# Kernel tuning notes

Hardware: AMD Instinct MI355X
Metric: run time of the kernel (lower is better)

The kernel has to match this reference:

```python
import jax, jax.numpy as jnp
import numpy as np
import math

B, H, N, L = 8, 512, 64, 4096

def setup_inputs() -> dict:
    key = jax.random.key(0)
    k = jax.random.split(key, 8)
    u = jax.random.normal(k[0], (B, H, L), dtype=jnp.float32)
    log_dt = jax.random.uniform(k[1], (H,), dtype=jnp.float32) * (math.log(0.1) - math.log(0.001)) + math.log(0.001)
    C_re = jax.random.normal(k[2], (H, N // 2), dtype=jnp.float32)
    C_im = jax.random.normal(k[3], (H, N // 2), dtype=jnp.float32)
    log_A_real = jnp.log(0.5 * jnp.ones((H, N // 2), dtype=jnp.float32))
    A_imag = math.pi * jnp.broadcast_to(jnp.arange(N // 2, dtype=jnp.float32), (H, N // 2))
    D = jax.random.normal(k[4], (H,), dtype=jnp.float32)
    # 1x1 conv H -> 2H (weights stored (2H, H)), PyTorch-like init scale 1/sqrt(H)
    s = 1.0 / math.sqrt(H)
    W = jax.random.uniform(k[5], (2 * H, H), dtype=jnp.float32, minval=-s, maxval=s)
    b = jax.random.uniform(k[6], (2 * H,), dtype=jnp.float32, minval=-s, maxval=s)
    return {"u": u, "log_dt": log_dt, "C_re": C_re, "C_im": C_im,
            "log_A_real": log_A_real, "A_imag": A_imag, "D": D, "W": W, "b": b}

def reference(u, log_dt, C_re, C_im, log_A_real, A_imag, D, W, b):
    Lq = u.shape[-1]
    dt = jnp.exp(log_dt)                       # (H,)
    C = C_re + 1j * C_im                       # (H, N/2)
    A = -jnp.exp(log_A_real) + 1j * A_imag     # (H, N/2)
    dtA = A * dt[:, None]                      # (H, N/2)
    # Vandermonde: exp(dtA * l) for l in [0, L)
    Kv = jnp.exp(dtA[:, :, None] * jnp.arange(Lq, dtype=jnp.float32))  # (H, N/2, L)
    Ck = C * (jnp.exp(dtA) - 1.0) / A          # (H, N/2)
    k = 2.0 * jnp.einsum('hn,hnl->hl', Ck, Kv).real  # (H, L)
    # FFT-based causal convolution with length-2L zero padding
    k_f = jnp.fft.rfft(k, n=2 * Lq)            # (H, L+1)
    u_f = jnp.fft.rfft(u, n=2 * Lq)            # (B, H, L+1)
    y = jnp.fft.irfft(u_f * k_f, n=2 * Lq)[..., :Lq]  # (B, H, L)
    y = y + u * D[:, None]
    y = jax.nn.gelu(y, approximate=False)      # nn.GELU default (erf)
    # 1x1 conv H -> 2H then GLU over channel dim (-2)
    z = jnp.einsum('oh,bhl->bol', W, y) + b[:, None]   # (B, 2H, L)
    a, g = jnp.split(z, 2, axis=-2)
    return a * jax.nn.sigmoid(g)               # (B, H, L)
```

## Files before the change

### kernel.cpp

```cpp
#include <hip/hip_runtime.h>
#include <hip/hip_bf16.h>
#include <math.h>

#define Bb 8
#define Hh 512
#define N2 32
#define Ll 4096
#define CH 256
#define NCH 16

#define KG_OFF  8388608
#define CKR_OFF (KG_OFF + 131072)
#define CKI_OFF (CKR_OFF + 16384)
#define W256R_OFF (CKI_OFF + 16384)
#define W256I_OFF (W256R_OFF + 16384)
#define WNHI_OFF 18874368u
#define WNLO_OFF 27525120u

typedef short bf16x8 __attribute__((ext_vector_type(8)));
typedef float f32x4  __attribute__((ext_vector_type(4)));

__device__ __forceinline__ float gelu_f(float x) {
    return 0.5f * x * (1.f + erff(x * 0.70710678118654752f));
}
__device__ __forceinline__ unsigned short f2bf(float f) {
    __hip_bfloat16 h = __float2bfloat16(f);
    return *reinterpret_cast<unsigned short*>(&h);
}
__device__ __forceinline__ float bf2f(unsigned short s) {
    return __uint_as_float(((unsigned int)s) << 16);
}

__global__ __launch_bounds__(256) void s4d_k1(
    const float* __restrict__ log_dt,
    const float* __restrict__ C_re,  const float* __restrict__ C_im,
    const float* __restrict__ log_A_real, const float* __restrict__ A_imag,
    const float* __restrict__ W,
    float* __restrict__ scratch, unsigned short* __restrict__ Wb,
    unsigned short* __restrict__ wnhi, unsigned short* __restrict__ wnlo,
    unsigned short* __restrict__ wnt)
{
    __shared__ __align__(16) float wLr[N2][257];
    __shared__ __align__(16) float wLi[N2][257];
    __shared__ float Ck2r[N2], Ck2i[N2];

    const int tid = threadIdx.x;
    const int h = blockIdx.x;

    {
        const int i4 = (blockIdx.x * 256 + tid) * 4;
        const float4 wv = *(const float4*)&W[i4];
        unsigned short o[4] = {f2bf(wv.x), f2bf(wv.y), f2bf(wv.z), f2bf(wv.w)};
        *(uint2*)&Wb[i4] = *(uint2*)o;
    }

    const float dt = expf(log_dt[h]);
    const int n = tid & 31, tq = tid >> 5;

    const float lar = log_A_real[h * N2 + n];
    const float Aim = A_imag[h * N2 + n];
    const float Are = -expf(lar);
    const float dar = Are * dt, dai = Aim * dt;

    float wr, wi;
    { float e = expf(dar); float sn, cs; sincosf(dai, &sn, &cs); wr = e * cs; wi = e * sn; }
    const float j0 = (float)(32 * tq + 1);
    float cr, ci;
    { float e = expf(dar * j0); float sn, cs; sincosf(dai * j0, &sn, &cs); cr = e * cs; ci = e * sn; }
    #pragma unroll 8
    for (int i = 0; i < 32; ++i) {
        const int j = 32 * tq + i;
        wLr[n][j] = cr; wLi[n][j] = ci;
        const float tr = cr * wr - ci * wi;
        ci = cr * wi + ci * wr; cr = tr;
    }

    if (tid < N2) {
        const float er = wr - 1.f, ei = wi;
        const float den = Are * Are + Aim * Aim;
        const float qr = (er * Are + ei * Aim) / den;
        const float qi = (ei * Are - er * Aim) / den;
        const float c_r = C_re[h * N2 + tid], c_i = C_im[h * N2 + tid];
        const float k2r = 2.f * (c_r * qr - c_i * qi);
        const float k2i = 2.f * (c_r * qi + c_i * qr);
        Ck2r[tid] = k2r; Ck2i[tid] = k2i;
        scratch[CKR_OFF + h * 32 + tid] = k2r;
        scratch[CKI_OFF + h * 32 + tid] = k2i;
    }
    __syncthreads();

    {
        const int t = tid;
        float kv = 0.f;
        if (t == 0) {
            #pragma unroll
            for (int m = 0; m < N2; ++m) kv += Ck2r[m];
        } else {
            #pragma unroll
            for (int m = 0; m < N2; ++m)
                kv += Ck2r[m] * wLr[m][t - 1] - Ck2i[m] * wLi[m][t - 1];
        }
        scratch[KG_OFF + h * CH + t] = kv;
    }

    {
        unsigned short* WH  = wnhi + (size_t)h * (64 * 264);
        unsigned short* WLo = wnlo + (size_t)h * (64 * 136);
        unsigned short* WT  = wnt  + (size_t)h * (257 * 64);

        for (int idx = tid; idx < 64 * 33; idx += 256) {
            const int r = idx / 33, g = idx - 33 * r;
            const float* src = (r & 1) ? wLi[r >> 1] : wLr[r >> 1];
            __align__(16) unsigned short o[8];
            #pragma unroll
            for (int jj = 0; jj < 8; ++jj) {
                const int j = 8 * g + jj;
                const float v = (j == 0) ? ((r & 1) ? 0.f : 1.f)
                              : (j <= 256 ? src[j - 1] : 0.f);
                o[jj] = f2bf(v);
            }
            *(uint4*)&WH[r * 264 + 8 * g] = *(const uint4*)o;
        }
        for (int idx = tid; idx < 64 * 17; idx += 256) {
            const int r = idx / 17, g = idx - 17 * r;
            const float* src = (r & 1) ? wLi[r >> 1] : wLr[r >> 1];
            __align__(16) unsigned short o[8];
            #pragma unroll
            for (int jj = 0; jj < 8; ++jj) {
                const int j = 8 * g + jj;
                const float v = (j == 0) ? ((r & 1) ? 0.f : 1.f)
                              : (j < 128 ? src[j - 1] : 0.f);
                o[jj] = f2bf(v - bf2f(f2bf(v)));
            }
            *(uint4*)&WLo[r * 136 + 8 * g] = *(const uint4*)o;
        }
        for (int idx = tid; idx < 257 * 8; idx += 256) {
            const int t = idx >> 3, g = idx & 7;
            __align__(16) unsigned short o[8];
            #pragma unroll
            for (int rr = 0; rr < 8; ++rr) {
                const int r = 8 * g + rr;
                const float v = (t == 0) ? ((r & 1) ? 0.f : 1.f)
                              : ((r & 1) ? wLi[r >> 1][t - 1] : wLr[r >> 1][t - 1]);
                o[rr] = f2bf(v);
            }
            *(uint4*)&WT[t * 64 + 8 * g] = *(const uint4*)o;
        }
        if (tid < N2) {
            scratch[W256R_OFF + h * 32 + tid] = wLr[tid][255];
            scratch[W256I_OFF + h * 32 + tid] = wLi[tid][255];
        }
    }
}

__global__ __launch_bounds__(256, 3) void s4d_k23(
    const float* __restrict__ u,
    const float* __restrict__ Dp,
    const float* scratch,
    const unsigned short* wnhi, const unsigned short* wnlo,
    const unsigned short* wnt,
    unsigned short* y_bf)
{
    __shared__ __align__(16) unsigned short uhi[16 * 264];
    __shared__ __align__(16) unsigned short ulo[16 * 264];
    __shared__ __align__(16) unsigned short khi[8 * 520];
    __shared__ __align__(16) unsigned short klo[8 * 520];
    __shared__ __align__(16) float Plds[64 * 20];
    __shared__ __align__(16) unsigned short CkAhi[16 * 72];
    __shared__ __align__(16) unsigned short CkAlo[16 * 72];

    const int tid = threadIdx.x;
    const int h = blockIdx.x & (Hh - 1);
    const int b = blockIdx.x >> 9;
    const int wv = tid >> 6;
    const int lane = tid & 63;
    const int l15 = lane & 15;
    const int quad = lane >> 4;

    {
        unsigned int* z1 = (unsigned int*)khi;
        unsigned int* z2 = (unsigned int*)klo;
        for (int i = tid; i < 2080; i += 256) { z1[i] = 0; z2[i] = 0; }
    }
    const float* ub = u + (size_t)(b * Hh + h) * Ll;
    #pragma unroll
    for (int q = 0; q < 4; ++q) {
        const int l = q * 1024 + tid * 4;
        const float4 v = *(const float4*)&ub[l];
        const int c = l >> 8, s = l & 255;
        const unsigned short h3 = f2bf(v.w), h2 = f2bf(v.z), h1 = f2bf(v.y), h0 = f2bf(v.x);
        uint2 dh;
        dh.x = (unsigned int)h3 | ((unsigned int)h2 << 16);
        dh.y = (unsigned int)h1 | ((unsigned int)h0 << 16);
        *(uint2*)&uhi[c * 264 + (252 - s)] = dh;
        uint2 dl;
        dl.x = (unsigned int)f2bf(v.w - bf2f(h3)) | ((unsigned int)f2bf(v.z - bf2f(h2)) << 16);
        dl.y = (unsigned int)f2bf(v.y - bf2f(h1)) | ((unsigned int)f2bf(v.x - bf2f(h0)) << 16);
        *(uint2*)&ulo[c * 264 + (252 - s)] = dl;
    }
    const float kval = scratch[KG_OFF + h * CH + tid];
    const unsigned short k_hi = f2bf(kval);
    const unsigned short k_lo = f2bf(kval - bf2f(k_hi));
    __syncthreads();

    #pragma unroll
    for (int r = 0; r < 8; ++r) {
        const int x = tid + 255 - r;
        khi[r * 520 + x] = k_hi;
        klo[r * 520 + x] = k_lo;
    }
    {
        const unsigned short* WH = wnhi + (size_t)h * (64 * 264);
        const unsigned short* WL = wnlo + (size_t)h * (64 * 136);
        f32x4 accP = {0.f, 0.f, 0.f, 0.f};
        const int wrow = 16 * wv + l15;
        #pragma unroll
        for (int j0 = 0; j0 < 256; j0 += 32) {
            const bf16x8 ah = *(const bf16x8*)&uhi[l15 * 264 + j0 + 8 * quad];
            const bf16x8 al = *(const bf16x8*)&ulo[l15 * 264 + j0 + 8 * quad];
            const bf16x8 wh = *(const bf16x8*)&WH[wrow * 264 + j0 + 8 * quad];
            accP = __builtin_amdgcn_mfma_f32_16x16x32_bf16(ah, wh, accP, 0, 0, 0);
            accP = __builtin_amdgcn_mfma_f32_16x16x32_bf16(al, wh, accP, 0, 0, 0);
            if (j0 < 128) {
                const bf16x8 wl = *(const bf16x8*)&WL[wrow * 136 + j0 + 8 * quad];
                accP = __builtin_amdgcn_mfma_f32_16x16x32_bf16(ah, wl, accP, 0, 0, 0);
            }
        }
        *(f32x4*)&Plds[wrow * 20 + 4 * quad] = accP;
    }
    __syncthreads();

    bf16x8 sf[8];
    {
        const unsigned short* WT = wnt + (size_t)h * (257 * 64);
        #pragma unroll
        for (int ks2 = 0; ks2 < 2; ++ks2)
            #pragma unroll
            for (int i = 0; i < 4; ++i) {
                const int tcol = 16 * (wv + 4 * i) + l15 + 1;
                sf[ks2 * 4 + i] = *(const bf16x8*)&WT[tcol * 64 + 32 * ks2 + 8 * quad];
            }
    }

    if (tid < 32) {
        const int n = tid;
        const float k2r = scratch[CKR_OFF + h * 32 + n];
        const float k2i = scratch[CKI_OFF + h * 32 + n];
        const float wCr = scratch[W256R_OFF + h * 32 + n];
        const float wCi = scratch[W256I_OFF + h * 32 + n];
        float sr = 0.f, si = 0.f;
        #pragma unroll
        for (int c = 0; c < NCH; ++c) {
            const float vr = k2r * sr - k2i * si;
            const float vi = -(k2r * si + k2i * sr);
            const unsigned short vrh = f2bf(vr), vih = f2bf(vi);
            *(unsigned int*)&CkAhi[c * 72 + 2 * n] =
                (unsigned int)vrh | ((unsigned int)vih << 16);
            *(unsigned int*)&CkAlo[c * 72 + 2 * n] =
                (unsigned int)f2bf(vr - bf2f(vrh)) |
                ((unsigned int)f2bf(vi - bf2f(vih)) << 16);
            const float pr = Plds[(2 * n) * 20 + c], pi = Plds[(2 * n + 1) * 20 + c];
            const float nr = wCr * sr - wCi * si + pr;
            si = wCr * si + wCi * sr + pi;
            sr = nr;
        }
    }

    f32x4 acc[4];
    #pragma unroll
    for (int i = 0; i < 4; ++i) acc[i] = (f32x4){0.f, 0.f, 0.f, 0.f};
    {
        const int r = lane & 7;
        const int roff = r * 520;
        const int half = ((lane >> 3) & 1) * 8;
        #pragma unroll
        for (int i = 0; i < 4; ++i) {
            const int nt = wv + 4 * i;
            const int jstart = (240 - 16 * nt) & ~31;
            for (int j0 = jstart; j0 < 256; j0 += 32) {
                const bf16x8 ah = *(const bf16x8*)&uhi[l15 * 264 + j0 + 8 * quad];
                const bf16x8 al = *(const bf16x8*)&ulo[l15 * 264 + j0 + 8 * quad];
                const int base = 16 * nt + j0 + 8 * quad + half;
                const bf16x8 bh = *(const bf16x8*)&khi[roff + base];
                const bf16x8 bl = *(const bf16x8*)&klo[roff + base];
                acc[i] = __builtin_amdgcn_mfma_f32_16x16x32_bf16(ah, bh, acc[i], 0, 0, 0);
                acc[i] = __builtin_amdgcn_mfma_f32_16x16x32_bf16(ah, bl, acc[i], 0, 0, 0);
                acc[i] = __builtin_amdgcn_mfma_f32_16x16x32_bf16(al, bh, acc[i], 0, 0, 0);
            }
        }
    }
    __syncthreads();

    #pragma unroll
    for (int ks2 = 0; ks2 < 2; ++ks2) {
        const int ks = 32 * ks2;
        const bf16x8 ah = *(const bf16x8*)&CkAhi[l15 * 72 + ks + 8 * quad];
        const bf16x8 al = *(const bf16x8*)&CkAlo[l15 * 72 + ks + 8 * quad];
        #pragma unroll
        for (int i = 0; i < 4; ++i) {
            acc[i] = __builtin_amdgcn_mfma_f32_16x16x32_bf16(ah, sf[ks2 * 4 + i], acc[i], 0, 0, 0);
            acc[i] = __builtin_amdgcn_mfma_f32_16x16x32_bf16(al, sf[ks2 * 4 + i], acc[i], 0, 0, 0);
        }
    }

    const float Dh = Dp[h];
    unsigned short* yo = y_bf + (size_t)(b * Hh + h) * Ll;
    #pragma unroll
    for (int i = 0; i < 4; ++i) {
        const int t = 16 * (wv + 4 * i) + l15;
        const int jrev = 255 - t;
        #pragma unroll
        for (int rr = 0; rr < 4; ++rr) {
            const int c = 4 * quad + rr;
            const float uu = bf2f(uhi[c * 264 + jrev]) + bf2f(ulo[c * 264 + jrev]);
            const float yv = acc[i][rr] + Dh * uu;
            yo[c * 256 + t] = f2bf(gelu_f(yv));
        }
    }
}

__global__ __launch_bounds__(256) void s4d_T(
    const unsigned short* y_bf, unsigned short* __restrict__ y_T)
{
    __shared__ unsigned short T[64][72];
    const int tid = threadIdx.x;
    const int b  = blockIdx.x >> 9;
    const int k0 = ((blockIdx.x >> 6) & 7) << 6;
    const int l0 = (blockIdx.x & 63) << 6;

    #pragma unroll
    for (int q = 0; q < 2; ++q) {
        const int idx = tid + 256 * q;
        const int kk = idx >> 3, lg = idx & 7;
        const uint4 v = *(const uint4*)&y_bf[((size_t)(b * Hh + k0 + kk)) * Ll + l0 + 8 * lg];
        const int gp = lg ^ ((kk >> 3) & 7);
        *(uint4*)&T[kk][8 * gp] = v;
    }
    __syncthreads();
    #pragma unroll
    for (int q = 0; q < 2; ++q) {
        const int idx = tid + 256 * q;
        const int ll = idx >> 3, kg = idx & 7;
        unsigned short o[8];
        #pragma unroll
        for (int j = 0; j < 8; ++j) {
            const int kr = 8 * kg + j;
            const int gp = (ll >> 3) ^ kg;
            o[j] = T[kr][8 * gp + (ll & 7)];
        }
        *(uint4*)&y_T[((size_t)(b * Ll + l0 + ll)) * Hh + k0 + 8 * kg] = *(uint4*)o;
    }
}

__global__ __launch_bounds__(256, 2) void s4d_s2(
    const unsigned short* __restrict__ yT,
    const unsigned short* __restrict__ Wb,
    const float* __restrict__ bias,
    float* __restrict__ out)
{
    __shared__ __align__(16) unsigned short Wlds[128 * 72];
    __shared__ __align__(16) unsigned short Ylds[128 * 72];

    const int tid = threadIdx.x;
    const int ct = blockIdx.x;
    const int mt = blockIdx.y;
    const int b  = ct >> 5;
    const int l0 = (ct & 31) << 7;
    const int m0 = mt << 6;

    const int wv = tid >> 6, lane = tid & 63;
    const int l15 = lane & 15, quad = lane >> 4;

    f32x4 accA[8], accG[8];
    #pragma unroll
    for (int j = 0; j < 8; ++j) {
        accA[j] = (f32x4){0.f, 0.f, 0.f, 0.f};
        accG[j] = (f32x4){0.f, 0.f, 0.f, 0.f};
    }

    for (int kk = 0; kk < Hh; kk += 64) {
        #pragma unroll
        for (int q = 0; q < 4; ++q) {
            const int idx = tid + 256 * q;
            const int rr = idx >> 3, kg = idx & 7;
            const int grow = m0 + rr + ((rr >> 6) * 448);
            *(uint4*)&Wlds[rr * 72 + 8 * kg] = *(const uint4*)&Wb[grow * Hh + kk + 8 * kg];
            *(uint4*)&Ylds[rr * 72 + 8 * kg] =
                *(const uint4*)&yT[((size_t)(b * Ll + l0 + rr)) * Hh + kk + 8 * kg];
        }
        __syncthreads();

        #pragma unroll
        for (int ks = 0; ks < 64; ks += 32) {
            const bf16x8 af = *(const bf16x8*)&Wlds[(16 * wv + l15) * 72 + ks + 8 * quad];
            const bf16x8 gf = *(const bf16x8*)&Wlds[(64 + 16 * wv + l15) * 72 + ks + 8 * quad];
            #pragma unroll
            for (int j = 0; j < 8; ++j) {
                const bf16x8 bfr = *(const bf16x8*)&Ylds[(16 * j + l15) * 72 + ks + 8 * quad];
                accA[j] = __builtin_amdgcn_mfma_f32_16x16x32_bf16(af, bfr, accA[j], 0, 0, 0);
                accG[j] = __builtin_amdgcn_mfma_f32_16x16x32_bf16(gf, bfr, accG[j], 0, 0, 0);
            }
        }
        __syncthreads();
    }

    const int mb = m0 + 16 * wv + 4 * quad;
    float bA[4], bG[4];
    #pragma unroll
    for (int rr = 0; rr < 4; ++rr) { bA[rr] = bias[mb + rr]; bG[rr] = bias[mb + rr + 512]; }

    #pragma unroll
    for (int j = 0; j < 8; ++j) {
        const int l = l0 + 16 * j + l15;
        #pragma unroll
        for (int rr = 0; rr < 4; ++rr) {
            const float a = accA[j][rr] + bA[rr];
            const float g = accG[j][rr] + bG[rr];
            out[((size_t)(b * Hh + mb + rr)) * Ll + l] = a / (1.f + expf(-g));
        }
    }
}

extern "C" void kernel_launch(void* const* d_in, const int* in_sizes, int n_in,
                              void* d_out, int out_size, void* d_ws, size_t ws_size,
                              hipStream_t stream)
{
    const float* u          = (const float*)d_in[0];
    const float* log_dt     = (const float*)d_in[1];
    const float* C_re       = (const float*)d_in[2];
    const float* C_im       = (const float*)d_in[3];
    const float* log_A_real = (const float*)d_in[4];
    const float* A_imag     = (const float*)d_in[5];
    const float* Dp         = (const float*)d_in[6];
    const float* W          = (const float*)d_in[7];
    const float* bias       = (const float*)d_in[8];

    float* out = (float*)d_out;
    float* scratch = (float*)d_out;
    unsigned short* y_bf = (unsigned short*)d_out;
    unsigned short* wnhi = (unsigned short*)d_out + WNHI_OFF;
    unsigned short* wnlo = (unsigned short*)d_out + WNLO_OFF;
    unsigned short* y_T  = (unsigned short*)d_ws;
    unsigned short* wnt  = (unsigned short*)d_ws;
    unsigned short* Wb   = (unsigned short*)((char*)d_ws + (32u << 20));

    s4d_k1<<<dim3(Hh), dim3(256), 0, stream>>>(
        log_dt, C_re, C_im, log_A_real, A_imag, W, scratch, Wb, wnhi, wnlo, wnt);
    s4d_k23<<<dim3(Bb * Hh), dim3(256), 0, stream>>>(
        u, Dp, scratch, wnhi, wnlo, wnt, y_bf);
    s4d_T<<<dim3(Bb * Hh), dim3(256), 0, stream>>>(y_bf, y_T);
    s4d_s2<<<dim3(256, 8), dim3(256), 0, stream>>>(y_T, Wb, bias, out);
}
```

Baseline: 265.0 us.

## Use direct global-to-LDS loads with XOR swizzle in GLU GEMM and remap conv blocks

The GLU GEMM kernel now loads W and y tiles with global_load_lds 16-byte direct transfers instead of staging through registers. It replaces the padded LDS layout with an XOR-swizzled unpadded one to avoid bank conflicts, and raises the occupancy hint from 2 to 4 blocks per CU. The conv kernel's block index is remapped so neighbouring blocks cover 8 batches for groups of 8 heads, which should improve L2 reuse of the per-head weights. The risk is that direct-to-LDS loads must complete before the barrier, and the swizzle must line up with the MFMA read pattern.

```diff
diff --git a/kernel.cpp b/kernel.cpp
--- a/kernel.cpp
+++ b/kernel.cpp
@@ -29,6 +29,11 @@
 }
 __device__ __forceinline__ float bf2f(unsigned short s) {
     return __uint_as_float(((unsigned int)s) << 16);
+}
+__device__ __forceinline__ void gl2lds16(const void* g, void* l) {
+    __builtin_amdgcn_global_load_lds(
+        (const __attribute__((address_space(1))) void*)g,
+        (__attribute__((address_space(3))) void*)l, 16, 0, 0);
 }
 
 __global__ __launch_bounds__(256) void s4d_k1(
@@ -170,8 +175,9 @@
     __shared__ __align__(16) unsigned short CkAlo[16 * 72];
 
     const int tid = threadIdx.x;
-    const int h = blockIdx.x & (Hh - 1);
-    const int b = blockIdx.x >> 9;
+    const int x = blockIdx.x;
+    const int h = ((x >> 6) << 3) | (x & 7);
+    const int b = (x >> 3) & 7;
     const int wv = tid >> 6;
     const int lane = tid & 63;
     const int l15 = lane & 15;
@@ -205,9 +211,9 @@
 
     #pragma unroll
     for (int r = 0; r < 8; ++r) {
-        const int x = tid + 255 - r;
-        khi[r * 520 + x] = k_hi;
-        klo[r * 520 + x] = k_lo;
+        const int x2 = tid + 255 - r;
+        khi[r * 520 + x2] = k_hi;
+        klo[r * 520 + x2] = k_lo;
     }
     {
         const unsigned short* WH = wnhi + (size_t)h * (64 * 264);
@@ -352,14 +358,14 @@
     }
 }
 
-__global__ __launch_bounds__(256, 2) void s4d_s2(
+__global__ __launch_bounds__(256, 4) void s4d_s2(
     const unsigned short* __restrict__ yT,
     const unsigned short* __restrict__ Wb,
     const float* __restrict__ bias,
     float* __restrict__ out)
 {
-    __shared__ __align__(16) unsigned short Wlds[128 * 72];
-    __shared__ __align__(16) unsigned short Ylds[128 * 72];
+    __shared__ __align__(16) unsigned short Wlds[128 * 64];
+    __shared__ __align__(16) unsigned short Ylds[128 * 64];
 
     const int tid = threadIdx.x;
     const int ct = blockIdx.x;
@@ -383,20 +389,24 @@
         for (int q = 0; q < 4; ++q) {
             const int idx = tid + 256 * q;
             const int rr = idx >> 3, kg = idx & 7;
+            const int sw = kg ^ (rr & 7);
             const int grow = m0 + rr + ((rr >> 6) * 448);
-            *(uint4*)&Wlds[rr * 72 + 8 * kg] = *(const uint4*)&Wb[grow * Hh + kk + 8 * kg];
-            *(uint4*)&Ylds[rr * 72 + 8 * kg] =
-                *(const uint4*)&yT[((size_t)(b * Ll + l0 + rr)) * Hh + kk + 8 * kg];
+            gl2lds16(&Wb[grow * Hh + kk + 8 * sw], &Wlds[8 * idx]);
+            gl2lds16(&yT[((size_t)(b * Ll + l0 + rr)) * Hh + kk + 8 * sw], &Ylds[8 * idx]);
         }
         __syncthreads();
 
         #pragma unroll
         for (int ks = 0; ks < 64; ks += 32) {
-            const bf16x8 af = *(const bf16x8*)&Wlds[(16 * wv + l15) * 72 + ks + 8 * quad];
-            const bf16x8 gf = *(const bf16x8*)&Wlds[(64 + 16 * wv + l15) * 72 + ks + 8 * quad];
+            const int c0 = (ks >> 3) + quad;
+            const int arow = 16 * wv + l15;
+            const bf16x8 af = *(const bf16x8*)&Wlds[arow * 64 + 8 * (c0 ^ (arow & 7))];
+            const int grow2 = 64 + arow;
+            const bf16x8 gf = *(const bf16x8*)&Wlds[grow2 * 64 + 8 * (c0 ^ (grow2 & 7))];
             #pragma unroll
             for (int j = 0; j < 8; ++j) {
-                const bf16x8 bfr = *(const bf16x8*)&Ylds[(16 * j + l15) * 72 + ks + 8 * quad];
+                const int brow = 16 * j + l15;
+                const bf16x8 bfr = *(const bf16x8*)&Ylds[brow * 64 + 8 * (c0 ^ (brow & 7))];
                 accA[j] = __builtin_amdgcn_mfma_f32_16x16x32_bf16(af, bfr, accA[j], 0, 0, 0);
                 accG[j] = __builtin_amdgcn_mfma_f32_16x16x32_bf16(gf, bfr, accG[j], 0, 0, 0);
             }
```

Result: faster. 242.3 us (-8.6%).
